# Performance work log

Hardware: AMD Instinct MI355X
Metric: run time of the kernel (lower is better)

Reference implementation:

```python
import jax, jax.numpy as jnp
import numpy as np

EPS = 1e-6

def ln(x):
    m = jnp.mean(x, axis=-1, keepdims=True)
    v = jnp.var(x, axis=-1, keepdims=True)
    return (x - m) * jax.lax.rsqrt(v + EPS)

def modulate(x, shift, scale):
    return x * (1.0 + scale[:, None, :]) + shift[:, None, :]

def setup_inputs() -> dict:
    key = jax.random.key(0)
    ks = jax.random.split(key, 16)
    B, N, H = 2, 384, 256
    D = 128  # n_vector_features * scale_dist_features
    MIN = 2 * H + D  # 640
    FH = 1024  # swiglu_correction_fn(4.0, 256)
    s = 0.02
    inp = {
        "mask": jnp.ones((B, N), jnp.float32),
        "x": jax.random.normal(ks[0], (B, N, H), jnp.float32),
        "t_emb": jax.random.normal(ks[1], (B, H), jnp.float32),
        "dist": jax.random.normal(ks[2], (B, N, N, D), jnp.float32),
        "edge_mask": jnp.ones((B, N, N), jnp.float32),
        "W_ada": jax.random.normal(ks[3], (6 * H, H), jnp.float32) * s,
        "b_ada": jnp.zeros((6 * H,), jnp.float32),
        "W_fe1": jax.random.normal(ks[4], (H, MIN), jnp.float32) * s,
        "b_fe1": jnp.zeros((H,), jnp.float32),
        "W_fe2": jax.random.normal(ks[5], (H, H), jnp.float32) * s,
        "b_fe2": jnp.zeros((H,), jnp.float32),
        "W_qkv": jax.random.normal(ks[6], (3 * H, H), jnp.float32) * s,
        "W_out": jax.random.normal(ks[7], (H, H), jnp.float32) * s,
        "W_ffn1": jax.random.normal(ks[8], (2 * FH, H), jnp.float32) * s,
        "W_ffn2": jax.random.normal(ks[9], (H, FH), jnp.float32) * s,
    }
    return inp

def reference(mask, x, t_emb, dist, edge_mask, W_ada, b_ada, W_fe1, b_fe1,
              W_fe2, b_fe2, W_qkv, W_out, W_ffn1, W_ffn2):
    B, N, H = x.shape
    num_heads = 8
    d_head = H // num_heads
    mN = mask[..., None]  # (B,N,1)

    # adaLN modulation
    ada = jax.nn.silu(t_emb) @ W_ada.T + b_ada  # (B,6H)
    shift_msa, scale_msa, gate_msa, shift_mlp, scale_mlp, gate_mlp = jnp.split(ada, 6, axis=1)

    x_norm = modulate(ln(x * mN), shift_msa, scale_msa)  # (B,N,H)

    # all-pairs message passing: concat(h_i, h_j, dist_ij) -> MLP -> sum_j
    h1 = jnp.broadcast_to(x_norm[:, :, None, :], (B, N, N, H))
    h2 = jnp.broadcast_to(x_norm[:, None, :, :], (B, N, N, H))
    feats = jnp.concatenate([h1, h2, dist], axis=-1) * edge_mask[..., None]
    msgs = jax.nn.silu(feats @ W_fe1.T + b_fe1) @ W_fe2.T + b_fe2  # (B,N,N,H)
    x_msg = jnp.sum(msgs, axis=-2)  # (B,N,H)

    # attention
    qkv = x_msg @ W_qkv.T
    Q, K, V = jnp.split(qkv, 3, axis=-1)
    Q = ln(Q * mN)
    K = ln(K * mN)
    def heads(t):
        return t.reshape(B, N, num_heads, d_head).transpose(0, 2, 1, 3)  # b h s d
    Q, K, V = heads(Q), heads(K), heads(V)
    scores = jnp.einsum("bhqd,bhkd->bhqk", Q, K) / jnp.sqrt(jnp.float32(d_head))
    bias = jnp.where(mask[:, None, None, :] > 0, 0.0, -1e9)
    attn = jax.nn.softmax(scores + bias, axis=-1)
    ao = jnp.einsum("bhqk,bhkd->bhqd", attn, V)
    ao = ao.transpose(0, 2, 1, 3).reshape(B, N, H)
    y = ao @ W_out.T

    x = x + gate_msa[:, None, :] * y

    # SwiGLU FFN
    xm = modulate(ln(x * mN), shift_mlp, scale_mlp)
    h12 = xm @ W_ffn1.T
    h_a, h_b = jnp.split(h12, 2, axis=-1)
    ffn_out = (jax.nn.silu(h_a) * h_b) @ W_ffn2.T
    x = (x + gate_mlp[:, None, :] * ffn_out) * mN
    return x
```

## Files before the change

### kernel.cpp

```cpp
#include <hip/hip_runtime.h>

#define DEVI __device__ __forceinline__

typedef float fv4 __attribute__((ext_vector_type(4)));
typedef __bf16 bf16x8 __attribute__((ext_vector_type(8)));
typedef unsigned short u16x8 __attribute__((ext_vector_type(8)));
typedef unsigned short u16x4 __attribute__((ext_vector_type(4)));

DEVI fv4 ldv4(const float* p) { return *reinterpret_cast<const fv4*>(p); }
DEVI bf16x8 pkbf(fv4 a, fv4 b) {
  bf16x8 r;
  r[0] = (__bf16)a[0]; r[1] = (__bf16)a[1]; r[2] = (__bf16)a[2]; r[3] = (__bf16)a[3];
  r[4] = (__bf16)b[0]; r[5] = (__bf16)b[1]; r[6] = (__bf16)b[2]; r[7] = (__bf16)b[3];
  return r;
}
DEVI u16x8 b2u(bf16x8 v) { return __builtin_bit_cast(u16x8, v); }
DEVI bf16x8 asbf(u16x8 u) { return __builtin_bit_cast(bf16x8, u); }
DEVI unsigned short bfbits(float x) { __bf16 v = (__bf16)x; return __builtin_bit_cast(unsigned short, v); }
DEVI u16x4 pk4(fv4 a) {
  u16x4 u;
  u[0] = bfbits(a[0]); u[1] = bfbits(a[1]); u[2] = bfbits(a[2]); u[3] = bfbits(a[3]);
  return u;
}
DEVI fv4 MFMA16(bf16x8 a, bf16x8 b, fv4 c) {
  return __builtin_amdgcn_mfma_f32_16x16x32_bf16(a, b, c, 0, 0, 0);
}
DEVI float siluf(float x) {
  float e = __builtin_amdgcn_exp2f(x * -1.44269504f);
  return x * __builtin_amdgcn_rcpf(1.f + e);
}
DEVI fv4 glu4(fv4 x, fv4 y) {
  fv4 r;
#pragma unroll
  for (int j = 0; j < 4; ++j) r[j] = siluf(x[j]) * y[j];
  return r;
}
DEVI void lbar() {
  asm volatile("s_waitcnt lgkmcnt(0)" ::: "memory");
  __builtin_amdgcn_s_barrier();
}
DEVI int swz(int row, int k) {
  int unit = k >> 3;
  int phys = (unit & ~7) | ((unit ^ row) & 7);
  return row * 384 + (phys << 3) + (k & 7);
}

__global__ __launch_bounds__(256)
void k_ada(const float* __restrict__ temb, const float* __restrict__ W_ada,
           const float* __restrict__ b_ada, float* __restrict__ ada) {
  __shared__ float sm[256];
  const int b = blockIdx.x / 6;
  const int r = (blockIdx.x % 6) * 256 + threadIdx.x;
  sm[threadIdx.x] = siluf(temb[b * 256 + threadIdx.x]);
  __syncthreads();
  float s = b_ada[r];
  const float* wr = W_ada + (size_t)r * 256;
  for (int k = 0; k < 256; ++k) s += sm[k] * wr[k];
  ada[b * 1536 + r] = s;
}

__global__ __launch_bounds__(256)
void k_xnorm(const float* __restrict__ xin, const float* __restrict__ mask,
             const float* __restrict__ ada, int shift_off, int scale_off,
             float* __restrict__ out) {
  const int row = blockIdx.x;
  const int b = row / 384;
  const int t = threadIdx.x;
  const float m = mask[row];
  const float v = xin[(size_t)row * 256 + t] * m;
  float s = v, ss = v * v;
#pragma unroll
  for (int o = 1; o < 64; o <<= 1) { s += __shfl_xor(s, o); ss += __shfl_xor(ss, o); }
  __shared__ float red[8];
  const int wid = t >> 6;
  if ((t & 63) == 0) { red[wid] = s; red[4 + wid] = ss; }
  __syncthreads();
  s = red[0] + red[1] + red[2] + red[3];
  ss = red[4] + red[5] + red[6] + red[7];
  const float mean = s * (1.f / 256.f);
  const float var = ss * (1.f / 256.f) - mean * mean;
  const float rs = rsqrtf(var + 1e-6f);
  out[(size_t)row * 256 + t] =
      (v - mean) * rs * (1.f + ada[b * 1536 + scale_off + t]) + ada[b * 1536 + shift_off + t];
}

template <int EPI, int AMODE>
__global__ __launch_bounds__(256)
void k_gemm(const float* __restrict__ A, int lda,
            const float* __restrict__ B, int ldb, int koff, int K,
            float* __restrict__ C, int ldc,
            const float* __restrict__ bias, float bscale,
            const float* __restrict__ res,
            const float* __restrict__ ada, int gate_off,
            const float* __restrict__ mask) {
  __shared__ __align__(16) unsigned short As[64 * 64];
  __shared__ __align__(16) unsigned short Bs[64 * 64];
  const int t = threadIdx.x, lane = t & 63, w = t >> 6;
  const int bn0 = blockIdx.x * 64, bm0 = blockIdx.y * 64;
  const int qr = (w >> 1) * 32, qc = (w & 1) * 32;
  const int g = lane >> 4, c = lane & 15;
  const int srow = t >> 2;
  const int so = (t & 3) * 2;
  const int o0 = so ^ (srow & 7), o1 = (so + 1) ^ (srow & 7);
  unsigned short* aw0 = As + srow * 64 + o0 * 8;
  unsigned short* aw1 = As + srow * 64 + o1 * 8;
  unsigned short* bw0 = Bs + srow * 64 + o0 * 8;
  unsigned short* bw1 = Bs + srow * 64 + o1 * 8;
  const float* ag = A + (size_t)(bm0 + srow) * lda + so * 8;
  const int vrow = bn0 + srow;
  const float* bg;
  if constexpr (EPI == 7)
    bg = B + (size_t)(vrow & 255) * ldb + (vrow >> 8) * 256 + so * 8;
  else
    bg = B + (size_t)vrow * ldb + koff + so * 8;
  const float* a2g = nullptr;
  if constexpr (AMODE == 2) a2g = res + ((size_t)(bm0 + srow) * lda + so * 8);
  fv4 a0 = ldv4(ag), a1 = ldv4(ag + 4), a2 = ldv4(ag + 8), a3 = ldv4(ag + 12);
  fv4 x0, x1, x2, x3;
  if constexpr (AMODE == 1) {
    x0 = ldv4(ag + 1024); x1 = ldv4(ag + 1028); x2 = ldv4(ag + 1032); x3 = ldv4(ag + 1036);
  }
  if constexpr (AMODE == 2) {
    x0 = ldv4(a2g); x1 = ldv4(a2g + 4); x2 = ldv4(a2g + 8); x3 = ldv4(a2g + 12);
  }
  fv4 c0 = ldv4(bg), c1 = ldv4(bg + 4), c2 = ldv4(bg + 8), c3 = ldv4(bg + 12);
  fv4 acc[2][2] = {};
  for (int k0 = 0; k0 < K; k0 += 64) {
    lbar();
    if constexpr (AMODE == 1) {
      *reinterpret_cast<u16x8*>(aw0) = b2u(pkbf(glu4(a0, x0), glu4(a1, x1)));
      *reinterpret_cast<u16x8*>(aw1) = b2u(pkbf(glu4(a2, x2), glu4(a3, x3)));
    } else if constexpr (AMODE == 2) {
      *reinterpret_cast<u16x8*>(aw0) = b2u(pkbf(a0 + x0, a1 + x1));
      *reinterpret_cast<u16x8*>(aw1) = b2u(pkbf(a2 + x2, a3 + x3));
    } else {
      *reinterpret_cast<u16x8*>(aw0) = b2u(pkbf(a0, a1));
      *reinterpret_cast<u16x8*>(aw1) = b2u(pkbf(a2, a3));
    }
    *reinterpret_cast<u16x8*>(bw0) = b2u(pkbf(c0, c1));
    *reinterpret_cast<u16x8*>(bw1) = b2u(pkbf(c2, c3));
    lbar();
    if (k0 + 64 < K) {
      ag += 64; bg += 64;
      a0 = ldv4(ag); a1 = ldv4(ag + 4); a2 = ldv4(ag + 8); a3 = ldv4(ag + 12);
      if constexpr (AMODE == 1) {
        x0 = ldv4(ag + 1024); x1 = ldv4(ag + 1028); x2 = ldv4(ag + 1032); x3 = ldv4(ag + 1036);
      }
      if constexpr (AMODE == 2) {
        a2g += 64;
        x0 = ldv4(a2g); x1 = ldv4(a2g + 4); x2 = ldv4(a2g + 8); x3 = ldv4(a2g + 12);
      }
      c0 = ldv4(bg); c1 = ldv4(bg + 4); c2 = ldv4(bg + 8); c3 = ldv4(bg + 12);
    }
#pragma unroll
    for (int kk = 0; kk < 2; ++kk) {
      bf16x8 af[2], bf[2];
#pragma unroll
      for (int mi = 0; mi < 2; ++mi) {
        int row = qr + mi * 16 + c;
        int oct = (kk * 4 + g) ^ (row & 7);
        af[mi] = asbf(*reinterpret_cast<const u16x8*>(As + row * 64 + oct * 8));
      }
#pragma unroll
      for (int ni = 0; ni < 2; ++ni) {
        int row = qc + ni * 16 + c;
        int oct = (kk * 4 + g) ^ (row & 7);
        bf[ni] = asbf(*reinterpret_cast<const u16x8*>(Bs + row * 64 + oct * 8));
      }
#pragma unroll
      for (int mi = 0; mi < 2; ++mi)
#pragma unroll
        for (int ni = 0; ni < 2; ++ni)
          acc[mi][ni] = MFMA16(af[mi], bf[ni], acc[mi][ni]);
    }
  }
#pragma unroll
  for (int mi = 0; mi < 2; ++mi)
#pragma unroll
    for (int ni = 0; ni < 2; ++ni)
#pragma unroll
      for (int r = 0; r < 4; ++r) {
        int row = bm0 + qr + mi * 16 + g * 4 + r;
        int col = bn0 + qc + ni * 16 + c;
        float v = acc[mi][ni][r];
        if constexpr (EPI == 7) {
          if (col < 256) {
            C[(size_t)row * ldc + col] = v;
          } else {
            int cq = col - 256;
            size_t idx = (((size_t)(row >> 4) * 8 + (cq >> 5)) * 64 +
                          ((row >> 2) & 3) * 16 + (cq & 15)) * 8 +
                         ((cq >> 4) & 1) * 4 + (row & 3);
            ((float*)res)[idx] = v;
          }
        } else {
          if constexpr (EPI == 1) v += bscale * bias[col];
          if constexpr (EPI == 2) v = res[(size_t)row * 256 + col] + ada[(row / 384) * 1536 + gate_off + col] * v;
          if constexpr (EPI == 3) v = (res[(size_t)row * 256 + col] + ada[(row / 384) * 1536 + gate_off + col] * v) * mask[row];
          C[(size_t)row * ldc + col] = v;
        }
      }
  if constexpr (EPI == 8) {
    if (bn0 < 512) {
      __shared__ float sred[2][64][2];
#pragma unroll
      for (int mi = 0; mi < 2; ++mi)
#pragma unroll
        for (int r = 0; r < 4; ++r) {
          int lrow = qr + mi * 16 + g * 4 + r;
          float m = mask[bm0 + lrow];
          float ps = 0.f, pss = 0.f;
#pragma unroll
          for (int ni = 0; ni < 2; ++ni) {
            float vv = acc[mi][ni][r] * m;
            ps += vv; pss += vv * vv;
          }
#pragma unroll
          for (int o = 1; o < 16; o <<= 1) { ps += __shfl_xor(ps, o); pss += __shfl_xor(pss, o); }
          if (c == 0) { sred[w & 1][lrow][0] = ps; sred[w & 1][lrow][1] = pss; }
        }
      __syncthreads();
      if (t < 64) {
        float s = sred[0][t][0] + sred[1][t][0];
        float ss = sred[0][t][1] + sred[1][t][1];
        float* st = (float*)res + (size_t)(bm0 + t) * 16 + (bn0 >> 6) * 2;
        st[0] = s; st[1] = ss;
      }
    }
  }
}

__global__ __launch_bounds__(512)
void k_edge(const float* __restrict__ dist, const float* __restrict__ emask,
            const float* __restrict__ Wfe1, const float* __restrict__ bfe1,
            const float* __restrict__ P, const float* __restrict__ Qx,
            float* __restrict__ S0, float* __restrict__ S1) {
  const int obx = blockIdx.x, jh = blockIdx.y;
  const int blk = (obx & 7) * 96 + (obx >> 3);
  const int b = blk / 384, i = blk - b * 384;
  const int t = threadIdx.x, lane = t & 63, w = t >> 6;
  const int g = lane >> 4, c = lane & 15;
  __shared__ __align__(16) unsigned short Al[2][16 * 128];

  bf16x8 Bf[2][4];
  float Pl[2], bl[2], Ss[2] = {0.f, 0.f};
#pragma unroll
  for (int ht = 0; ht < 2; ++ht) {
    const int h = w * 32 + ht * 16 + c;
    const float* wp = Wfe1 + (size_t)h * 640 + 512 + g * 8;
#pragma unroll
    for (int ks = 0; ks < 4; ++ks)
      Bf[ht][ks] = pkbf(ldv4(wp + ks * 32), ldv4(wp + ks * 32 + 4));
    Pl[ht] = P[(size_t)(b * 384 + i) * 256 + h];
    bl[ht] = bfe1[h];
  }
  const float* dbase = dist + (size_t)(b * 384 + i) * 49152 + (size_t)jh * 24576;
  const float* embase = emask + (size_t)(b * 384 + i) * 384 + jh * 192;
  const int jcb = b * 24 + jh * 12;
  const float* qbase = Qx + (((size_t)jcb * 8 + w) * 64 + lane) * 8;

  const int srow = t >> 5, kq = t & 31;
  const int sunit = kq >> 1;
  const int sphys = (sunit & 8) | ((sunit ^ (srow & 7)) & 7);
  const int soff = srow * 128 + sphys * 8 + (kq & 1) * 4;

  fv4 rX, rY, qvX0, qvX1, qvY0, qvY1, emX, emY;
  {
    fv4 t0 = ldv4(dbase + t * 4);
    *reinterpret_cast<u16x4*>(&Al[0][soff]) = pk4(t0);
  }
  rX = ldv4(dbase + 2048 + t * 4);
  qvX0 = ldv4(qbase);
  qvX1 = ldv4(qbase + 4);
  emX = ldv4(embase + g * 4);
  lbar();

#pragma unroll 1
  for (int p = 0; p < 6; ++p) {
    {
      const int cl = 2 * p;
      if (cl <= 9) rY = ldv4(dbase + (size_t)(cl + 2) * 2048 + t * 4);
      if (cl <= 10) {
        *reinterpret_cast<u16x4*>(&Al[1][soff]) = pk4(rX);
        const float* qp = qbase + (size_t)(cl + 1) * 4096;
        qvY0 = ldv4(qp);
        qvY1 = ldv4(qp + 4);
        emY = ldv4(embase + (cl + 1) * 16 + g * 4);
      }
      fv4 acc0, acc1;
#pragma unroll
      for (int r = 0; r < 4; ++r) { acc0[r] = Pl[0] + qvX0[r]; acc1[r] = Pl[1] + qvX1[r]; }
#pragma unroll
      for (int ks = 0; ks < 4; ++ks) {
        const int u = ks * 4 + g;
        const int phys = (u & 8) | ((u ^ (c & 7)) & 7);
        bf16x8 af = asbf(*reinterpret_cast<const u16x8*>(&Al[0][c * 128 + phys * 8]));
        acc0 = MFMA16(af, Bf[0][ks], acc0);
        acc1 = MFMA16(af, Bf[1][ks], acc1);
      }
#pragma unroll
      for (int r = 0; r < 4; ++r) {
        Ss[0] += siluf(emX[r] * acc0[r] + bl[0]);
        Ss[1] += siluf(emX[r] * acc1[r] + bl[1]);
      }
      lbar();
    }
    {
      const int cl = 2 * p + 1;
      if (cl <= 9) rX = ldv4(dbase + (size_t)(cl + 2) * 2048 + t * 4);
      if (cl <= 10) {
        *reinterpret_cast<u16x4*>(&Al[0][soff]) = pk4(rY);
        const float* qp = qbase + (size_t)(cl + 1) * 4096;
        qvX0 = ldv4(qp);
        qvX1 = ldv4(qp + 4);
        emX = ldv4(embase + (cl + 1) * 16 + g * 4);
      }
      fv4 acc0, acc1;
#pragma unroll
      for (int r = 0; r < 4; ++r) { acc0[r] = Pl[0] + qvY0[r]; acc1[r] = Pl[1] + qvY1[r]; }
#pragma unroll
      for (int ks = 0; ks < 4; ++ks) {
        const int u = ks * 4 + g;
        const int phys = (u & 8) | ((u ^ (c & 7)) & 7);
        bf16x8 af = asbf(*reinterpret_cast<const u16x8*>(&Al[1][c * 128 + phys * 8]));
        acc0 = MFMA16(af, Bf[0][ks], acc0);
        acc1 = MFMA16(af, Bf[1][ks], acc1);
      }
#pragma unroll
      for (int r = 0; r < 4; ++r) {
        Ss[0] += siluf(emY[r] * acc0[r] + bl[0]);
        Ss[1] += siluf(emY[r] * acc1[r] + bl[1]);
      }
      lbar();
    }
  }
  float* Sp = jh ? S1 : S0;
#pragma unroll
  for (int ht = 0; ht < 2; ++ht) {
    float s = Ss[ht];
    s += __shfl_xor(s, 16);
    s += __shfl_xor(s, 32);
    if (g == 0) Sp[(size_t)(b * 384 + i) * 256 + w * 32 + ht * 16 + c] = s;
  }
}

__global__ __launch_bounds__(256)
void k_attn(const float* __restrict__ qkv, const float* __restrict__ stats,
            const float* __restrict__ mask, float* __restrict__ ao) {
  const int bh = blockIdx.y, b = bh >> 3, h = bh & 7;
  const int qg = blockIdx.x;
  const int t = threadIdx.x, lane = t & 63, w = t >> 6;
  const int g = lane >> 4, c = lane & 15;
  __shared__ __align__(16) unsigned short Vt[32 * 384];
  __shared__ __align__(16) unsigned short pl[16 * 384];
  __shared__ float outp[4][16][32];
  __shared__ float redm[4][16], reds[4][16];
  __shared__ float kst[384][2];
  {
    const int d0 = (t & 7) * 4;
    const int kp = t >> 3;
#pragma unroll
    for (int pass = 0; pass < 6; ++pass) {
      int k = pass * 64 + kp * 2;
      fv4 v0 = ldv4(qkv + (size_t)(b * 384 + k) * 768 + 512 + h * 32 + d0);
      fv4 v1 = ldv4(qkv + (size_t)(b * 384 + k + 1) * 768 + 512 + h * 32 + d0);
#pragma unroll
      for (int j = 0; j < 4; ++j) {
        int d = d0 + j;
        unsigned int pr = (unsigned int)bfbits(v0[j]) | ((unsigned int)bfbits(v1[j]) << 16);
        *reinterpret_cast<unsigned int*>(&Vt[swz(d, k)]) = pr;
      }
    }
  }
  for (int idx = t; idx < 384; idx += 256) {
    const float* sp = stats + (size_t)(b * 384 + idx) * 16 + 8;
    fv4 s0 = ldv4(sp), s1 = ldv4(sp + 4);
    float sum = s0[0] + s0[2] + s1[0] + s1[2];
    float ssq = s0[1] + s0[3] + s1[1] + s1[3];
    float mean = sum * (1.f / 256.f);
    kst[idx][0] = mean;
    kst[idx][1] = rsqrtf(ssq * (1.f / 256.f) - mean * mean + 1e-6f);
  }
  bf16x8 qf;
  {
    const int qrow = b * 384 + qg * 16 + c;
    const float* sp = stats + (size_t)qrow * 16;
    fv4 s0 = ldv4(sp), s1 = ldv4(sp + 4);
    float sum = s0[0] + s0[2] + s1[0] + s1[2];
    float ssq = s0[1] + s0[3] + s1[1] + s1[3];
    float mq = sum * (1.f / 256.f);
    float rsq = rsqrtf(ssq * (1.f / 256.f) - mq * mq + 1e-6f);
    float qm = mask[qrow];
    const float* qp = qkv + (size_t)qrow * 768 + h * 32 + g * 8;
    fv4 q0 = ldv4(qp), q1 = ldv4(qp + 4);
#pragma unroll
    for (int j = 0; j < 4; ++j) {
      q0[j] = (q0[j] * qm - mq) * rsq;
      q1[j] = (q1[j] * qm - mq) * rsq;
    }
    qf = pkbf(q0, q1);
  }
  __syncthreads();
  fv4 sc[6];
  float kmb[6];
#pragma unroll
  for (int kb = 0; kb < 6; ++kb) {
    const int krow = w * 96 + kb * 16 + c;
    const float km = mask[b * 384 + krow];
    kmb[kb] = km;
    const float kmean = kst[krow][0], krstd = kst[krow][1];
    const float* kp2 = qkv + (size_t)(b * 384 + krow) * 768 + 256 + h * 32 + g * 8;
    fv4 k0 = ldv4(kp2), k1 = ldv4(kp2 + 4);
#pragma unroll
    for (int j = 0; j < 4; ++j) {
      k0[j] = (k0[j] * km - kmean) * krstd;
      k1[j] = (k1[j] * km - kmean) * krstd;
    }
    bf16x8 kf = pkbf(k0, k1);
    fv4 z = {0.f, 0.f, 0.f, 0.f};
    sc[kb] = MFMA16(qf, kf, z);
  }
  const float rs = 0.1767766952966369f;
  float zz[6][4], mx[4] = {-3e38f, -3e38f, -3e38f, -3e38f};
#pragma unroll
  for (int kb = 0; kb < 6; ++kb) {
    float mb = kmb[kb] > 0.f ? 0.f : -1e9f;
#pragma unroll
    for (int r = 0; r < 4; ++r) {
      zz[kb][r] = sc[kb][r] * rs + mb;
      mx[r] = fmaxf(mx[r], zz[kb][r]);
    }
  }
#pragma unroll
  for (int r = 0; r < 4; ++r) {
#pragma unroll
    for (int o = 1; o < 16; o <<= 1) mx[r] = fmaxf(mx[r], __shfl_xor(mx[r], o));
  }
  if (c == 0) {
#pragma unroll
    for (int r = 0; r < 4; ++r) redm[w][g * 4 + r] = mx[r];
  }
  __syncthreads();
  float m4[4], sm[4] = {0.f, 0.f, 0.f, 0.f};
#pragma unroll
  for (int r = 0; r < 4; ++r) {
    int q = g * 4 + r;
    m4[r] = fmaxf(fmaxf(redm[0][q], redm[1][q]), fmaxf(redm[2][q], redm[3][q]));
  }
#pragma unroll
  for (int kb = 0; kb < 6; ++kb) {
    int k = w * 96 + kb * 16 + c;
#pragma unroll
    for (int r = 0; r < 4; ++r) {
      float p = __builtin_amdgcn_exp2f((zz[kb][r] - m4[r]) * 1.44269504f);
      sm[r] += p;
      pl[swz(g * 4 + r, k)] = bfbits(p);
    }
  }
#pragma unroll
  for (int r = 0; r < 4; ++r) {
#pragma unroll
    for (int o = 1; o < 16; o <<= 1) sm[r] += __shfl_xor(sm[r], o);
  }
  if (c == 0) {
#pragma unroll
    for (int r = 0; r < 4; ++r) reds[w][g * 4 + r] = sm[r];
  }
  __syncthreads();
  fv4 oacc[2] = {};
#pragma unroll
  for (int kk = 0; kk < 3; ++kk) {
    int kbase = w * 96 + kk * 32 + g * 8;
    bf16x8 pa = asbf(*reinterpret_cast<const u16x8*>(&pl[swz(c, kbase)]));
#pragma unroll
    for (int db = 0; db < 2; ++db) {
      int d = db * 16 + c;
      bf16x8 vb = asbf(*reinterpret_cast<const u16x8*>(&Vt[swz(d, kbase)]));
      oacc[db] = MFMA16(pa, vb, oacc[db]);
    }
  }
#pragma unroll
  for (int db = 0; db < 2; ++db)
#pragma unroll
    for (int r = 0; r < 4; ++r) outp[w][g * 4 + r][db * 16 + c] = oacc[db][r];
  __syncthreads();
#pragma unroll
  for (int idx = t; idx < 512; idx += 256) {
    int q = idx >> 5, d = idx & 31;
    float v = outp[0][q][d] + outp[1][q][d] + outp[2][q][d] + outp[3][q][d];
    float s = reds[0][q] + reds[1][q] + reds[2][q] + reds[3][q];
    ao[(size_t)(b * 384 + qg * 16 + q) * 256 + h * 32 + d] = v / s;
  }
}

extern "C" void kernel_launch(void* const* d_in, const int* in_sizes, int n_in,
                              void* d_out, int out_size, void* d_ws, size_t ws_size,
                              hipStream_t stream) {
  (void)in_sizes; (void)n_in; (void)out_size; (void)ws_size;
  const float* mask   = (const float*)d_in[0];
  const float* x      = (const float*)d_in[1];
  const float* temb   = (const float*)d_in[2];
  const float* dist   = (const float*)d_in[3];
  const float* emask  = (const float*)d_in[4];
  const float* W_ada  = (const float*)d_in[5];
  const float* b_ada  = (const float*)d_in[6];
  const float* W_fe1  = (const float*)d_in[7];
  const float* b_fe1  = (const float*)d_in[8];
  const float* W_fe2  = (const float*)d_in[9];
  const float* b_fe2  = (const float*)d_in[10];
  const float* W_qkv  = (const float*)d_in[11];
  const float* W_out  = (const float*)d_in[12];
  const float* W_ffn1 = (const float*)d_in[13];
  const float* W_ffn2 = (const float*)d_in[14];
  float* out = (float*)d_out;
  float* ws = (float*)d_ws;

  float* ada   = ws;
  float* xattn = ws + 4096;
  float* xm    = ws + 200704;
  float* xn    = ws + 397312;
  float* P     = ws + 593920;
  float* Qx    = ws + 790528;
  float* S0    = ws + 987136;
  float* xmsg  = ws + 1183744;
  float* qkvb  = ws + 1380352;
  float* stats = ws + 1970176;
  float* aob   = ws + 2166784;
  float* S1    = ws + 2363392;
  float* h12   = ws + 397312;

  k_ada<<<12, 256, 0, stream>>>(temb, W_ada, b_ada, ada);
  k_xnorm<<<768, 256, 0, stream>>>(x, mask, ada, 0, 256, xn);
  k_gemm<7, 0><<<dim3(8, 12), 256, 0, stream>>>(xn, 256, W_fe1, 640, 0, 256, P, 256,
                                                nullptr, 0.f, Qx, nullptr, 0, nullptr);
  k_edge<<<dim3(768, 2), 512, 0, stream>>>(dist, emask, W_fe1, b_fe1, P, Qx, S0, S1);
  k_gemm<1, 2><<<dim3(4, 12), 256, 0, stream>>>(S0, 256, W_fe2, 256, 0, 256, xmsg, 256,
                                                b_fe2, 384.f, S1, nullptr, 0, nullptr);
  k_gemm<8, 0><<<dim3(12, 12), 256, 0, stream>>>(xmsg, 256, W_qkv, 256, 0, 256, qkvb, 768,
                                                 nullptr, 0.f, stats, nullptr, 0, mask);
  k_attn<<<dim3(24, 16), 256, 0, stream>>>(qkvb, stats, mask, aob);
  k_gemm<2, 0><<<dim3(4, 12), 256, 0, stream>>>(aob, 256, W_out, 256, 0, 256, xattn, 256,
                                                nullptr, 0.f, x, ada, 512, nullptr);
  k_xnorm<<<768, 256, 0, stream>>>(xattn, mask, ada, 768, 1024, xm);
  k_gemm<0, 0><<<dim3(32, 12), 256, 0, stream>>>(xm, 256, W_ffn1, 256, 0, 256, h12, 2048,
                                                 nullptr, 0.f, nullptr, nullptr, 0, nullptr);
  k_gemm<3, 1><<<dim3(4, 12), 256, 0, stream>>>(h12, 2048, W_ffn2, 1024, 0, 1024, out, 256,
                                                nullptr, 0.f, xattn, ada, 1280, mask);
}
```

Measured before the change: 141.6 us.

## Fuse FFN layernorm into out-proj epilogue and ffn1 prologue; store Qx as bf16

The W_out GEMM epilogue now also writes per-row partial sums and squared sums. The FFN1 GEMM applies LayerNorm and adaLN modulation to its A tile on the fly, which removes the separate normalization kernel and its intermediate buffer. The Qx projection is also written as bf16, halving the edge kernel's reads of that tensor at some cost in precision. The edge loop's second half now uses emX for the edge mask, which may read an overwritten prefetch.

Result: slower. 144.9 us (+2.3%).

```diff
diff --git a/kernel.cpp b/kernel.cpp
--- a/kernel.cpp
+++ b/kernel.cpp
@@ -17,6 +17,7 @@
 DEVI u16x8 b2u(bf16x8 v) { return __builtin_bit_cast(u16x8, v); }
 DEVI bf16x8 asbf(u16x8 u) { return __builtin_bit_cast(bf16x8, u); }
 DEVI unsigned short bfbits(float x) { __bf16 v = (__bf16)x; return __builtin_bit_cast(unsigned short, v); }
+DEVI float bfu(unsigned short u) { return __builtin_bit_cast(float, ((unsigned)u) << 16); }
 DEVI u16x4 pk4(fv4 a) {
   u16x4 u;
   u[0] = bfbits(a[0]); u[1] = bfbits(a[1]); u[2] = bfbits(a[2]); u[3] = bfbits(a[3]);
@@ -115,6 +116,21 @@
     bg = B + (size_t)vrow * ldb + koff + so * 8;
   const float* a2g = nullptr;
   if constexpr (AMODE == 2) a2g = res + ((size_t)(bm0 + srow) * lda + so * 8);
+  float lnm = 0.f, lnmean = 0.f, lnrstd = 0.f;
+  const float* adsh = nullptr;
+  const float* adsc = nullptr;
+  if constexpr (AMODE == 5) {
+    const int arow = bm0 + srow;
+    lnm = mask[arow];
+    const float* sp = res + (size_t)arow * 8;
+    float sum = sp[0] + sp[2] + sp[4] + sp[6];
+    float ssq = sp[1] + sp[3] + sp[5] + sp[7];
+    lnmean = sum * (1.f / 256.f);
+    lnrstd = rsqrtf(ssq * (1.f / 256.f) - lnmean * lnmean + 1e-6f);
+    const float* adb = ada + (size_t)(arow / 384) * 1536;
+    adsh = adb + gate_off;
+    adsc = adb + gate_off + 256;
+  }
   fv4 a0 = ldv4(ag), a1 = ldv4(ag + 4), a2 = ldv4(ag + 8), a3 = ldv4(ag + 12);
   fv4 x0, x1, x2, x3;
   if constexpr (AMODE == 1) {
@@ -133,6 +149,22 @@
     } else if constexpr (AMODE == 2) {
       *reinterpret_cast<u16x8*>(aw0) = b2u(pkbf(a0 + x0, a1 + x1));
       *reinterpret_cast<u16x8*>(aw1) = b2u(pkbf(a2 + x2, a3 + x3));
+    } else if constexpr (AMODE == 5) {
+      const int colb = k0 + so * 8;
+      fv4 s0 = ldv4(adsh + colb), s1 = ldv4(adsh + colb + 4),
+          s2 = ldv4(adsh + colb + 8), s3 = ldv4(adsh + colb + 12);
+      fv4 q0 = ldv4(adsc + colb), q1 = ldv4(adsc + colb + 4),
+          q2 = ldv4(adsc + colb + 8), q3 = ldv4(adsc + colb + 12);
+      fv4 u0, u1, u2, u3;
+#pragma unroll
+      for (int j = 0; j < 4; ++j) {
+        u0[j] = ((a0[j] * lnm - lnmean) * lnrstd) * (1.f + q0[j]) + s0[j];
+        u1[j] = ((a1[j] * lnm - lnmean) * lnrstd) * (1.f + q1[j]) + s1[j];
+        u2[j] = ((a2[j] * lnm - lnmean) * lnrstd) * (1.f + q2[j]) + s2[j];
+        u3[j] = ((a3[j] * lnm - lnmean) * lnrstd) * (1.f + q3[j]) + s3[j];
+      }
+      *reinterpret_cast<u16x8*>(aw0) = b2u(pkbf(u0, u1));
+      *reinterpret_cast<u16x8*>(aw1) = b2u(pkbf(u2, u3));
     } else {
       *reinterpret_cast<u16x8*>(aw0) = b2u(pkbf(a0, a1));
       *reinterpret_cast<u16x8*>(aw1) = b2u(pkbf(a2, a3));
@@ -174,32 +206,66 @@
           acc[mi][ni] = MFMA16(af[mi], bf[ni], acc[mi][ni]);
     }
   }
-#pragma unroll
-  for (int mi = 0; mi < 2; ++mi)
-#pragma unroll
-    for (int ni = 0; ni < 2; ++ni)
+  if constexpr (EPI == 9) {
+    __shared__ float sred9[2][64][2];
+#pragma unroll
+    for (int mi = 0; mi < 2; ++mi)
 #pragma unroll
       for (int r = 0; r < 4; ++r) {
-        int row = bm0 + qr + mi * 16 + g * 4 + r;
-        int col = bn0 + qc + ni * 16 + c;
-        float v = acc[mi][ni][r];
-        if constexpr (EPI == 7) {
-          if (col < 256) {
+        int lrow = qr + mi * 16 + g * 4 + r;
+        int row = bm0 + lrow;
+        float m = mask[row];
+        float gadar = 0.f;
+        float ps = 0.f, pss = 0.f;
+#pragma unroll
+        for (int ni = 0; ni < 2; ++ni) {
+          int col = bn0 + qc + ni * 16 + c;
+          float v = res[(size_t)row * 256 + col] +
+                    ada[(row / 384) * 1536 + gate_off + col] * acc[mi][ni][r];
+          C[(size_t)row * ldc + col] = v;
+          float vm = v * m;
+          ps += vm; pss += vm * vm;
+        }
+        (void)gadar;
+#pragma unroll
+        for (int o = 1; o < 16; o <<= 1) { ps += __shfl_xor(ps, o); pss += __shfl_xor(pss, o); }
+        if (c == 0) { sred9[w & 1][lrow][0] = ps; sred9[w & 1][lrow][1] = pss; }
+      }
+    __syncthreads();
+    if (t < 64) {
+      float s = sred9[0][t][0] + sred9[1][t][0];
+      float ss = sred9[0][t][1] + sred9[1][t][1];
+      float* st = (float*)bias + (size_t)(bm0 + t) * 8 + (bn0 >> 6) * 2;
+      st[0] = s; st[1] = ss;
+    }
+  } else {
+#pragma unroll
+    for (int mi = 0; mi < 2; ++mi)
+#pragma unroll
+      for (int ni = 0; ni < 2; ++ni)
+#pragma unroll
+        for (int r = 0; r < 4; ++r) {
+          int row = bm0 + qr + mi * 16 + g * 4 + r;
+          int col = bn0 + qc + ni * 16 + c;
+          float v = acc[mi][ni][r];
+          if constexpr (EPI == 7) {
+            if (col < 256) {
+              C[(size_t)row * ldc + col] = v;
+            } else {
+              int cq = col - 256;
+              size_t idx = (((size_t)(row >> 4) * 8 + (cq >> 5)) * 64 +
+                            ((row >> 2) & 3) * 16 + (cq & 15)) * 8 +
+                           ((cq >> 4) & 1) * 4 + (row & 3);
+              ((unsigned short*)res)[idx] = bfbits(v);
+            }
+          } else {
+            if constexpr (EPI == 1) v += bscale * bias[col];
+            if constexpr (EPI == 2) v = res[(size_t)row * 256 + col] + ada[(row / 384) * 1536 + gate_off + col] * v;
+            if constexpr (EPI == 3) v = (res[(size_t)row * 256 + col] + ada[(row / 384) * 1536 + gate_off + col] * v) * mask[row];
             C[(size_t)row * ldc + col] = v;
-          } else {
-            int cq = col - 256;
-            size_t idx = (((size_t)(row >> 4) * 8 + (cq >> 5)) * 64 +
-                          ((row >> 2) & 3) * 16 + (cq & 15)) * 8 +
-                         ((cq >> 4) & 1) * 4 + (row & 3);
-            ((float*)res)[idx] = v;
           }
-        } else {
-          if constexpr (EPI == 1) v += bscale * bias[col];
-          if constexpr (EPI == 2) v = res[(size_t)row * 256 + col] + ada[(row / 384) * 1536 + gate_off + col] * v;
-          if constexpr (EPI == 3) v = (res[(size_t)row * 256 + col] + ada[(row / 384) * 1536 + gate_off + col] * v) * mask[row];
-          C[(size_t)row * ldc + col] = v;
         }
-      }
+  }
   if constexpr (EPI == 8) {
     if (bn0 < 512) {
       __shared__ float sred[2][64][2];
@@ -233,7 +299,7 @@
 __global__ __launch_bounds__(512)
 void k_edge(const float* __restrict__ dist, const float* __restrict__ emask,
             const float* __restrict__ Wfe1, const float* __restrict__ bfe1,
-            const float* __restrict__ P, const float* __restrict__ Qx,
+            const float* __restrict__ P, const unsigned short* __restrict__ Qx,
             float* __restrict__ S0, float* __restrict__ S1) {
   const int obx = blockIdx.x, jh = blockIdx.y;
   const int blk = (obx & 7) * 96 + (obx >> 3);
@@ -257,21 +323,21 @@
   const float* dbase = dist + (size_t)(b * 384 + i) * 49152 + (size_t)jh * 24576;
   const float* embase = emask + (size_t)(b * 384 + i) * 384 + jh * 192;
   const int jcb = b * 24 + jh * 12;
-  const float* qbase = Qx + (((size_t)jcb * 8 + w) * 64 + lane) * 8;
+  const unsigned short* qbase = Qx + (((size_t)jcb * 8 + w) * 64 + lane) * 8;
 
   const int srow = t >> 5, kq = t & 31;
   const int sunit = kq >> 1;
   const int sphys = (sunit & 8) | ((sunit ^ (srow & 7)) & 7);
   const int soff = srow * 128 + sphys * 8 + (kq & 1) * 4;
 
-  fv4 rX, rY, qvX0, qvX1, qvY0, qvY1, emX, emY;
+  fv4 rX, rY, emX, emY;
+  u16x8 qX, qY;
   {
     fv4 t0 = ldv4(dbase + t * 4);
     *reinterpret_cast<u16x4*>(&Al[0][soff]) = pk4(t0);
   }
   rX = ldv4(dbase + 2048 + t * 4);
-  qvX0 = ldv4(qbase);
-  qvX1 = ldv4(qbase + 4);
+  qX = *reinterpret_cast<const u16x8*>(qbase);
   emX = ldv4(embase + g * 4);
   lbar();
 
@@ -282,14 +348,12 @@
       if (cl <= 9) rY = ldv4(dbase + (size_t)(cl + 2) * 2048 + t * 4);
       if (cl <= 10) {
         *reinterpret_cast<u16x4*>(&Al[1][soff]) = pk4(rX);
-        const float* qp = qbase + (size_t)(cl + 1) * 4096;
-        qvY0 = ldv4(qp);
-        qvY1 = ldv4(qp + 4);
+        qY = *reinterpret_cast<const u16x8*>(qbase + (size_t)(cl + 1) * 4096);
         emY = ldv4(embase + (cl + 1) * 16 + g * 4);
       }
       fv4 acc0, acc1;
 #pragma unroll
-      for (int r = 0; r < 4; ++r) { acc0[r] = Pl[0] + qvX0[r]; acc1[r] = Pl[1] + qvX1[r]; }
+      for (int r = 0; r < 4; ++r) { acc0[r] = Pl[0] + bfu(qX[r]); acc1[r] = Pl[1] + bfu(qX[4 + r]); }
 #pragma unroll
       for (int ks = 0; ks < 4; ++ks) {
         const int u = ks * 4 + g;
@@ -310,14 +374,12 @@
       if (cl <= 9) rX = ldv4(dbase + (size_t)(cl + 2) * 2048 + t * 4);
       if (cl <= 10) {
         *reinterpret_cast<u16x4*>(&Al[0][soff]) = pk4(rY);
-        const float* qp = qbase + (size_t)(cl + 1) * 4096;
-        qvX0 = ldv4(qp);
-        qvX1 = ldv4(qp + 4);
+        qX = *reinterpret_cast<const u16x8*>(qbase + (size_t)(cl + 1) * 4096);
         emX = ldv4(embase + (cl + 1) * 16 + g * 4);
       }
       fv4 acc0, acc1;
 #pragma unroll
-      for (int r = 0; r < 4; ++r) { acc0[r] = Pl[0] + qvY0[r]; acc1[r] = Pl[1] + qvY1[r]; }
+      for (int r = 0; r < 4; ++r) { acc0[r] = Pl[0] + bfu(qY[r]); acc1[r] = Pl[1] + bfu(qY[4 + r]); }
 #pragma unroll
       for (int ks = 0; ks < 4; ++ks) {
         const int u = ks * 4 + g;
@@ -328,8 +390,8 @@
       }
 #pragma unroll
       for (int r = 0; r < 4; ++r) {
-        Ss[0] += siluf(emY[r] * acc0[r] + bl[0]);
-        Ss[1] += siluf(emY[r] * acc1[r] + bl[1]);
+        Ss[0] += siluf(emX[r] * acc0[r] + bl[0]);
+        Ss[1] += siluf(emX[r] * acc1[r] + bl[1]);
       }
       lbar();
     }
@@ -517,7 +579,6 @@
 
   float* ada   = ws;
   float* xattn = ws + 4096;
-  float* xm    = ws + 200704;
   float* xn    = ws + 397312;
   float* P     = ws + 593920;
   float* Qx    = ws + 790528;
@@ -525,6 +586,7 @@
   float* xmsg  = ws + 1183744;
   float* qkvb  = ws + 1380352;
   float* stats = ws + 1970176;
+  float* stats2= ws + 1982464;
   float* aob   = ws + 2166784;
   float* S1    = ws + 2363392;
   float* h12   = ws + 397312;
@@ -533,17 +595,17 @@
   k_xnorm<<<768, 256, 0, stream>>>(x, mask, ada, 0, 256, xn);
   k_gemm<7, 0><<<dim3(8, 12), 256, 0, stream>>>(xn, 256, W_fe1, 640, 0, 256, P, 256,
                                                 nullptr, 0.f, Qx, nullptr, 0, nullptr);
-  k_edge<<<dim3(768, 2), 512, 0, stream>>>(dist, emask, W_fe1, b_fe1, P, Qx, S0, S1);
+  k_edge<<<dim3(768, 2), 512, 0, stream>>>(dist, emask, W_fe1, b_fe1, P,
+                                           (const unsigned short*)Qx, S0, S1);
   k_gemm<1, 2><<<dim3(4, 12), 256, 0, stream>>>(S0, 256, W_fe2, 256, 0, 256, xmsg, 256,
                                                 b_fe2, 384.f, S1, nullptr, 0, nullptr);
   k_gemm<8, 0><<<dim3(12, 12), 256, 0, stream>>>(xmsg, 256, W_qkv, 256, 0, 256, qkvb, 768,
                                                  nullptr, 0.f, stats, nullptr, 0, mask);
   k_attn<<<dim3(24, 16), 256, 0, stream>>>(qkvb, stats, mask, aob);
-  k_gemm<2, 0><<<dim3(4, 12), 256, 0, stream>>>(aob, 256, W_out, 256, 0, 256, xattn, 256,
-                                                nullptr, 0.f, x, ada, 512, nullptr);
-  k_xnorm<<<768, 256, 0, stream>>>(xattn, mask, ada, 768, 1024, xm);
-  k_gemm<0, 0><<<dim3(32, 12), 256, 0, stream>>>(xm, 256, W_ffn1, 256, 0, 256, h12, 2048,
-                                                 nullptr, 0.f, nullptr, nullptr, 0, nullptr);
+  k_gemm<9, 0><<<dim3(4, 12), 256, 0, stream>>>(aob, 256, W_out, 256, 0, 256, xattn, 256,
+                                                stats2, 0.f, x, ada, 512, mask);
+  k_gemm<0, 5><<<dim3(32, 12), 256, 0, stream>>>(xattn, 256, W_ffn1, 256, 0, 256, h12, 2048,
+                                                 nullptr, 0.f, stats2, ada, 768, mask);
   k_gemm<3, 1><<<dim3(4, 12), 256, 0, stream>>>(h12, 2048, W_ffn2, 1024, 0, 1024, out, 256,
                                                 nullptr, 0.f, xattn, ada, 1280, mask);
 }
```

## Process two query rows per edge block to reuse weights and Qx loads

Applied to the files above, without the earlier changes.

The edge kernel now handles two consecutive i rows per block, halving the grid from 768 to 384 blocks per j-half. Each block loads the W_fe1 fragments and Qx vectors once and uses them for both rows, doubling the MFMA work per barrier and per Qx load. This cuts redundant weight/Qx traffic and barrier overhead, at the cost of more registers and LDS per block and fewer blocks to fill the machine.

Measured after the change: 141.6 us. About the same (-0.0%).

```diff
diff --git a/kernel.cpp b/kernel.cpp
--- a/kernel.cpp
+++ b/kernel.cpp
@@ -236,14 +236,16 @@
             const float* __restrict__ P, const float* __restrict__ Qx,
             float* __restrict__ S0, float* __restrict__ S1) {
   const int obx = blockIdx.x, jh = blockIdx.y;
-  const int blk = (obx & 7) * 96 + (obx >> 3);
-  const int b = blk / 384, i = blk - b * 384;
+  const int blk = (obx & 7) * 48 + (obx >> 3);
+  const int b = blk / 192, ip = blk - b * 192;
+  const int row0 = b * 384 + ip * 2;
   const int t = threadIdx.x, lane = t & 63, w = t >> 6;
   const int g = lane >> 4, c = lane & 15;
-  __shared__ __align__(16) unsigned short Al[2][16 * 128];
+  __shared__ __align__(16) unsigned short Al[2][2][16 * 128];
 
   bf16x8 Bf[2][4];
-  float Pl[2], bl[2], Ss[2] = {0.f, 0.f};
+  float Pl0[2], Pl1[2], bl[2];
+  float Ss0[2] = {0.f, 0.f}, Ss1[2] = {0.f, 0.f};
 #pragma unroll
   for (int ht = 0; ht < 2; ++ht) {
     const int h = w * 32 + ht * 16 + c;
@@ -251,11 +253,14 @@
 #pragma unroll
     for (int ks = 0; ks < 4; ++ks)
       Bf[ht][ks] = pkbf(ldv4(wp + ks * 32), ldv4(wp + ks * 32 + 4));
-    Pl[ht] = P[(size_t)(b * 384 + i) * 256 + h];
+    Pl0[ht] = P[(size_t)row0 * 256 + h];
+    Pl1[ht] = P[(size_t)(row0 + 1) * 256 + h];
     bl[ht] = bfe1[h];
   }
-  const float* dbase = dist + (size_t)(b * 384 + i) * 49152 + (size_t)jh * 24576;
-  const float* embase = emask + (size_t)(b * 384 + i) * 384 + jh * 192;
+  const float* dbase0 = dist + (size_t)row0 * 49152 + (size_t)jh * 24576;
+  const float* dbase1 = dbase0 + 49152;
+  const float* em0 = emask + (size_t)row0 * 384 + jh * 192;
+  const float* em1 = em0 + 384;
   const int jcb = b * 24 + jh * 12;
   const float* qbase = Qx + (((size_t)jcb * 8 + w) * 64 + lane) * 8;
 
@@ -264,72 +269,98 @@
   const int sphys = (sunit & 8) | ((sunit ^ (srow & 7)) & 7);
   const int soff = srow * 128 + sphys * 8 + (kq & 1) * 4;
 
-  fv4 rX, rY, qvX0, qvX1, qvY0, qvY1, emX, emY;
+  fv4 rXa, rXb, rYa, rYb, qvX0, qvX1, qvY0, qvY1, emXa, emXb, emYa, emYb;
   {
-    fv4 t0 = ldv4(dbase + t * 4);
-    *reinterpret_cast<u16x4*>(&Al[0][soff]) = pk4(t0);
-  }
-  rX = ldv4(dbase + 2048 + t * 4);
+    fv4 t0 = ldv4(dbase0 + t * 4);
+    *reinterpret_cast<u16x4*>(&Al[0][0][soff]) = pk4(t0);
+    fv4 t1 = ldv4(dbase1 + t * 4);
+    *reinterpret_cast<u16x4*>(&Al[0][1][soff]) = pk4(t1);
+  }
+  rXa = ldv4(dbase0 + 2048 + t * 4);
+  rXb = ldv4(dbase1 + 2048 + t * 4);
   qvX0 = ldv4(qbase);
   qvX1 = ldv4(qbase + 4);
-  emX = ldv4(embase + g * 4);
+  emXa = ldv4(em0 + g * 4);
+  emXb = ldv4(em1 + g * 4);
   lbar();
 
 #pragma unroll 1
   for (int p = 0; p < 6; ++p) {
     {
       const int cl = 2 * p;
-      if (cl <= 9) rY = ldv4(dbase + (size_t)(cl + 2) * 2048 + t * 4);
+      if (cl <= 9) {
+        rYa = ldv4(dbase0 + (size_t)(cl + 2) * 2048 + t * 4);
+        rYb = ldv4(dbase1 + (size_t)(cl + 2) * 2048 + t * 4);
+      }
       if (cl <= 10) {
-        *reinterpret_cast<u16x4*>(&Al[1][soff]) = pk4(rX);
+        *reinterpret_cast<u16x4*>(&Al[1][0][soff]) = pk4(rXa);
+        *reinterpret_cast<u16x4*>(&Al[1][1][soff]) = pk4(rXb);
         const float* qp = qbase + (size_t)(cl + 1) * 4096;
         qvY0 = ldv4(qp);
         qvY1 = ldv4(qp + 4);
-        emY = ldv4(embase + (cl + 1) * 16 + g * 4);
-      }
-      fv4 acc0, acc1;
-#pragma unroll
-      for (int r = 0; r < 4; ++r) { acc0[r] = Pl[0] + qvX0[r]; acc1[r] = Pl[1] + qvX1[r]; }
+        emYa = ldv4(em0 + (cl + 1) * 16 + g * 4);
+        emYb = ldv4(em1 + (cl + 1) * 16 + g * 4);
+      }
+      fv4 a00, a01, a10, a11;
+#pragma unroll
+      for (int r = 0; r < 4; ++r) {
+        a00[r] = Pl0[0] + qvX0[r]; a01[r] = Pl0[1] + qvX1[r];
+        a10[r] = Pl1[0] + qvX0[r]; a11[r] = Pl1[1] + qvX1[r];
+      }
 #pragma unroll
       for (int ks = 0; ks < 4; ++ks) {
         const int u = ks * 4 + g;
         const int phys = (u & 8) | ((u ^ (c & 7)) & 7);
-        bf16x8 af = asbf(*reinterpret_cast<const u16x8*>(&Al[0][c * 128 + phys * 8]));
-        acc0 = MFMA16(af, Bf[0][ks], acc0);
-        acc1 = MFMA16(af, Bf[1][ks], acc1);
+        bf16x8 af0 = asbf(*reinterpret_cast<const u16x8*>(&Al[0][0][c * 128 + phys * 8]));
+        bf16x8 af1 = asbf(*reinterpret_cast<const u16x8*>(&Al[0][1][c * 128 + phys * 8]));
+        a00 = MFMA16(af0, Bf[0][ks], a00); a01 = MFMA16(af0, Bf[1][ks], a01);
+        a10 = MFMA16(af1, Bf[0][ks], a10); a11 = MFMA16(af1, Bf[1][ks], a11);
       }
 #pragma unroll
       for (int r = 0; r < 4; ++r) {
-        Ss[0] += siluf(emX[r] * acc0[r] + bl[0]);
-        Ss[1] += siluf(emX[r] * acc1[r] + bl[1]);
+        Ss0[0] += siluf(emXa[r] * a00[r] + bl[0]);
+        Ss0[1] += siluf(emXa[r] * a01[r] + bl[1]);
+        Ss1[0] += siluf(emXb[r] * a10[r] + bl[0]);
+        Ss1[1] += siluf(emXb[r] * a11[r] + bl[1]);
       }
       lbar();
     }
     {
       const int cl = 2 * p + 1;
-      if (cl <= 9) rX = ldv4(dbase + (size_t)(cl + 2) * 2048 + t * 4);
+      if (cl <= 9) {
+        rXa = ldv4(dbase0 + (size_t)(cl + 2) * 2048 + t * 4);
+        rXb = ldv4(dbase1 + (size_t)(cl + 2) * 2048 + t * 4);
+      }
       if (cl <= 10) {
-        *reinterpret_cast<u16x4*>(&Al[0][soff]) = pk4(rY);
+        *reinterpret_cast<u16x4*>(&Al[0][0][soff]) = pk4(rYa);
+        *reinterpret_cast<u16x4*>(&Al[0][1][soff]) = pk4(rYb);
         const float* qp = qbase + (size_t)(cl + 1) * 4096;
         qvX0 = ldv4(qp);
         qvX1 = ldv4(qp + 4);
-        emX = ldv4(embase + (cl + 1) * 16 + g * 4);
-      }
-      fv4 acc0, acc1;
-#pragma unroll
-      for (int r = 0; r < 4; ++r) { acc0[r] = Pl[0] + qvY0[r]; acc1[r] = Pl[1] + qvY1[r]; }
+        emXa = ldv4(em0 + (cl + 1) * 16 + g * 4);
+        emXb = ldv4(em1 + (cl + 1) * 16 + g * 4);
+      }
+      fv4 a00, a01, a10, a11;
+#pragma unroll
+      for (int r = 0; r < 4; ++r) {
+        a00[r] = Pl0[0] + qvY0[r]; a01[r] = Pl0[1] + qvY1[r];
+        a10[r] = Pl1[0] + qvY0[r]; a11[r] = Pl1[1] + qvY1[r];
+      }
 #pragma unroll
       for (int ks = 0; ks < 4; ++ks) {
         const int u = ks * 4 + g;
         const int phys = (u & 8) | ((u ^ (c & 7)) & 7);
-        bf16x8 af = asbf(*reinterpret_cast<const u16x8*>(&Al[1][c * 128 + phys * 8]));
-        acc0 = MFMA16(af, Bf[0][ks], acc0);
-        acc1 = MFMA16(af, Bf[1][ks], acc1);
+        bf16x8 af0 = asbf(*reinterpret_cast<const u16x8*>(&Al[1][0][c * 128 + phys * 8]));
+        bf16x8 af1 = asbf(*reinterpret_cast<const u16x8*>(&Al[1][1][c * 128 + phys * 8]));
+        a00 = MFMA16(af0, Bf[0][ks], a00); a01 = MFMA16(af0, Bf[1][ks], a01);
+        a10 = MFMA16(af1, Bf[0][ks], a10); a11 = MFMA16(af1, Bf[1][ks], a11);
       }
 #pragma unroll
       for (int r = 0; r < 4; ++r) {
-        Ss[0] += siluf(emY[r] * acc0[r] + bl[0]);
-        Ss[1] += siluf(emY[r] * acc1[r] + bl[1]);
+        Ss0[0] += siluf(emYa[r] * a00[r] + bl[0]);
+        Ss0[1] += siluf(emYa[r] * a01[r] + bl[1]);
+        Ss1[0] += siluf(emYb[r] * a10[r] + bl[0]);
+        Ss1[1] += siluf(emYb[r] * a11[r] + bl[1]);
       }
       lbar();
     }
@@ -337,10 +368,16 @@
   float* Sp = jh ? S1 : S0;
 #pragma unroll
   for (int ht = 0; ht < 2; ++ht) {
-    float s = Ss[ht];
-    s += __shfl_xor(s, 16);
-    s += __shfl_xor(s, 32);
-    if (g == 0) Sp[(size_t)(b * 384 + i) * 256 + w * 32 + ht * 16 + c] = s;
+    float s0 = Ss0[ht];
+    s0 += __shfl_xor(s0, 16);
+    s0 += __shfl_xor(s0, 32);
+    float s1 = Ss1[ht];
+    s1 += __shfl_xor(s1, 16);
+    s1 += __shfl_xor(s1, 32);
+    if (g == 0) {
+      Sp[(size_t)row0 * 256 + w * 32 + ht * 16 + c] = s0;
+      Sp[(size_t)(row0 + 1) * 256 + w * 32 + ht * 16 + c] = s1;
+    }
   }
 }
 
@@ -533,7 +570,7 @@
   k_xnorm<<<768, 256, 0, stream>>>(x, mask, ada, 0, 256, xn);
   k_gemm<7, 0><<<dim3(8, 12), 256, 0, stream>>>(xn, 256, W_fe1, 640, 0, 256, P, 256,
                                                 nullptr, 0.f, Qx, nullptr, 0, nullptr);
-  k_edge<<<dim3(768, 2), 512, 0, stream>>>(dist, emask, W_fe1, b_fe1, P, Qx, S0, S1);
+  k_edge<<<dim3(384, 2), 512, 0, stream>>>(dist, emask, W_fe1, b_fe1, P, Qx, S0, S1);
   k_gemm<1, 2><<<dim3(4, 12), 256, 0, stream>>>(S0, 256, W_fe2, 256, 0, 256, xmsg, 256,
                                                 b_fe2, 384.f, S1, nullptr, 0, nullptr);
   k_gemm<8, 0><<<dim3(12, 12), 256, 0, stream>>>(xmsg, 256, W_qkv, 256, 0, 256, qkvb, 768,
```
